# Optimization experiments

Measured on AMD Instinct MI355X. Metric: run time of the kernel, lower is better.

The kernel has to match this reference:

```python
import jax, jax.numpy as jnp
import numpy as np
from jax import lax

D_MODEL = 2048
D_STATE = 16
D_CONV = 4
B_SZ = 2
T_LEN = 2048


def setup_inputs() -> dict:
    key = jax.random.key(0)
    ks = jax.random.split(key, 8)
    x = jax.random.normal(ks[0], (B_SZ, T_LEN, D_MODEL), dtype=jnp.float32)
    h = jnp.zeros((B_SZ, D_MODEL, D_STATE), dtype=jnp.float32)
    norm_w = jnp.ones((D_MODEL,), dtype=jnp.float32)
    in_proj_w = jax.random.normal(ks[1], (2 * D_MODEL, D_MODEL), dtype=jnp.float32) * (D_MODEL ** -0.5)
    conv_w = jax.random.normal(ks[2], (D_MODEL, 1, D_CONV), dtype=jnp.float32) * 0.5
    conv_b = jnp.zeros((D_MODEL,), dtype=jnp.float32)
    x_proj_w = jax.random.normal(ks[3], (D_MODEL + 2 * D_STATE, D_MODEL), dtype=jnp.float32) * (D_MODEL ** -0.5)
    A_log = jnp.broadcast_to(jnp.log(jnp.arange(1, D_STATE + 1, dtype=jnp.float32))[None, :], (D_MODEL, D_STATE)).copy()
    D = jnp.ones((D_MODEL,), dtype=jnp.float32)
    out_proj_w = jax.random.normal(ks[4], (D_MODEL, D_MODEL), dtype=jnp.float32) * (D_MODEL ** -0.5)
    return {"x": x, "h": h, "norm_w": norm_w, "in_proj_w": in_proj_w,
            "conv_w": conv_w, "conv_b": conv_b, "x_proj_w": x_proj_w,
            "A_log": A_log, "D": D, "out_proj_w": out_proj_w}


def _rmsnorm(x, w, eps=1e-6):
    ms = jnp.mean(jnp.square(x.astype(jnp.float32)), axis=-1, keepdims=True)
    return (x * lax.rsqrt(ms + eps).astype(x.dtype)) * w.astype(x.dtype)


def reference(x, h, norm_w, in_proj_w, conv_w, conv_b, x_proj_w, A_log, D, out_proj_w):
    B, T, d_model = x.shape
    d_state = A_log.shape[1]
    residual = x
    x_normed = _rmsnorm(x, norm_w)
    xz = x_normed @ in_proj_w.T                      # (B, T, 2*d_model)
    x_branch, z = jnp.split(xz, 2, axis=-1)
    # depthwise causal conv1d: torch pads both sides by d_conv-1 then slices [:T],
    # equivalent to left-pad-only causal conv.
    xc = x_branch.transpose(0, 2, 1)                 # (B, d_model, T)
    xc = lax.conv_general_dilated(
        xc, conv_w, window_strides=(1,), padding=[(D_CONV - 1, 0)],
        dimension_numbers=("NCH", "OIH", "NCH"), feature_group_count=d_model)
    xc = xc + conv_b[None, :, None]
    x_ssm = jax.nn.silu(xc.transpose(0, 2, 1))       # (B, T, d_model)

    # SSM core
    proj = x_ssm @ x_proj_w.T                        # (B, T, d_model + 2*d_state)
    delta_raw = proj[..., :d_model]
    B_in = proj[..., d_model:d_model + d_state]
    C_in = proj[..., d_model + d_state:]
    delta = jax.nn.softplus(delta_raw)               # (B, T, d_model)
    A = -jnp.exp(A_log.astype(jnp.float32))          # (d_model, d_state)

    def step(h_c, inp):
        d_t, b_t, c_t, x_t = inp                     # (B,dm) (B,ds) (B,ds) (B,dm)
        A_bar = jnp.exp(d_t[:, :, None] * A[None])   # (B, dm, ds)
        h_c = A_bar * h_c + (d_t * x_t)[:, :, None] * b_t[:, None, :]
        y_t = jnp.einsum("bdn,bn->bd", h_c, c_t) + D * x_t
        return h_c, y_t

    xs = (delta.transpose(1, 0, 2), B_in.transpose(1, 0, 2),
          C_in.transpose(1, 0, 2), x_ssm.transpose(1, 0, 2))
    h_new, ys = lax.scan(step, h.astype(x.dtype), xs)
    y = ys.transpose(1, 0, 2)                        # (B, T, d_model)

    y = y * jax.nn.silu(z)
    out = residual + y @ out_proj_w.T
    return out, lax.stop_gradient(h_new)
```

## Files before the change

kernel.cpp:

```cpp
#include <hip/hip_runtime.h>
#include <cstdint>
#include <cstddef>


typedef __bf16 bf16_t;
typedef __attribute__((ext_vector_type(8))) __bf16 bf16x8;
typedef __attribute__((ext_vector_type(4))) __bf16 bf16x4;
typedef __attribute__((ext_vector_type(4))) float f32x4;

#define D_MODEL 2048
#define D_STATE 16
#define B_SZ 2
#define T_LEN 2048
#define N_ROWS (B_SZ * T_LEN)
#define N_PAD  2176
#define N_CHUNK 32
#define L_CHUNK (T_LEN / N_CHUNK)
#define LOG2E 1.4426950408889634f
#define KT 64
#define PANEL 32768

__device__ __forceinline__ size_t swz_idx(int row, int col) {
    return ((size_t)((row >> 4) * KT + (col >> 5)) << 9)
         + (size_t)(((row & 15) + (((col & 31) >> 3) << 4)) << 3) + (col & 7);
}

__global__ __launch_bounds__(256) void cast_weights(
    const float* __restrict__ w_in, const float* __restrict__ w_x,
    const float* __restrict__ w_out,
    bf16_t* __restrict__ W1s, bf16_t* __restrict__ W2s, bf16_t* __restrict__ W3s)
{
    int wv   = blockIdx.x * 4 + (threadIdx.x >> 6);
    int lane = threadIdx.x & 63;
    const float* src; bf16_t* dst; int nrows; int tile;
    if (wv < 16384)      { src = w_in;  dst = W1s; tile = wv;         nrows = 4096; }
    else if (wv < 25088) { src = w_x;   dst = W2s; tile = wv - 16384; nrows = 2080; }
    else                 { src = w_out; dst = W3s; tile = wv - 25088; nrows = 2048; }
    int r16 = tile >> 6, kt = tile & 63;
    int row = r16 * 16 + (lane & 15);
    int k0  = kt * 32 + (lane >> 4) * 8;
    f32x4 v0 = {0.f, 0.f, 0.f, 0.f}, v1 = v0;
    if (row < nrows) {
        v0 = *(const f32x4*)&src[(size_t)row * 2048 + k0];
        v1 = *(const f32x4*)&src[(size_t)row * 2048 + k0 + 4];
    }
    bf16x4 lo = __builtin_convertvector(v0, bf16x4);
    bf16x4 hi = __builtin_convertvector(v1, bf16x4);
    bf16x8 o;
    #pragma unroll
    for (int e = 0; e < 4; ++e) { o[e] = lo[e]; o[e + 4] = hi[e]; }
    *(bf16x8*)(dst + (size_t)tile * 512 + lane * 8) = o;
}

__global__ __launch_bounds__(256) void rmsnorm_swz(
    const float* __restrict__ x, const float* __restrict__ w,
    bf16_t* __restrict__ xn)
{
    int r16 = blockIdx.x;
    int tid = threadIdx.x;
    int wave = tid >> 6, lane = tid & 63;
    __shared__ float sc[16];
    #pragma unroll
    for (int rr = 0; rr < 4; ++rr) {
        int row = r16 * 16 + wave * 4 + rr;
        const float* xr = x + (size_t)row * 2048;
        float ss = 0.f;
        for (int i = lane * 4; i < 2048; i += 256) {
            f32x4 v = *(const f32x4*)&xr[i];
            ss += v[0]*v[0] + v[1]*v[1] + v[2]*v[2] + v[3]*v[3];
        }
        #pragma unroll
        for (int o = 32; o > 0; o >>= 1) ss += __shfl_down(ss, o, 64);
        if (lane == 0) sc[wave * 4 + rr] = rsqrtf(ss * (1.f / 2048.f) + 1e-6f);
    }
    __syncthreads();
    const size_t base = (size_t)r16 * PANEL;
    int m = lane & 15;
    int row = r16 * 16 + m;
    float s = sc[m];
    const float* xr = x + (size_t)row * 2048;
    for (int c = 0; c < 16; ++c) {
        int f  = (c * 256 + tid) * 8;
        int kt = f >> 9;
        int k  = kt * 32 + (lane >> 4) * 8;
        f32x4 v0 = *(const f32x4*)&xr[k];
        f32x4 v1 = *(const f32x4*)&xr[k + 4];
        f32x4 w0 = *(const f32x4*)&w[k];
        f32x4 w1 = *(const f32x4*)&w[k + 4];
        bf16x8 o;
        #pragma unroll
        for (int e = 0; e < 4; ++e) {
            o[e]     = (bf16_t)(v0[e] * s * w0[e]);
            o[e + 4] = (bf16_t)(v1[e] * s * w1[e]);
        }
        *(bf16x8*)(xn + base + f) = o;
    }
}

template<int MODE>
__global__ __launch_bounds__(256) void gemm_bt(
    const bf16_t* __restrict__ A, const bf16_t* __restrict__ B,
    float* __restrict__ out0, bf16_t* __restrict__ out1,
    const float* __restrict__ add)
{
    __shared__ __align__(16) float cs[32 * 132];
    const int tid = threadIdx.x;
    const int bm = blockIdx.x, bn = blockIdx.y;
    const int lane = tid & 63;
    const int wave = tid >> 6;
    const int wn = (wave >> 1) * 64;
    const int fr = lane & 15;
    const int quad = lane >> 4;

    const bf16_t* aB = A + (((size_t)(bm * 8 + (wave & 1) * 4) * KT) << 9) + lane * 8;
    const bf16_t* bB = B + (((size_t)(bn * 8 + (wave >> 1) * 4) * KT) << 9) + lane * 8;

    f32x4 acc[4][4];
    #pragma unroll
    for (int i = 0; i < 4; ++i)
        #pragma unroll
        for (int j = 0; j < 4; ++j) acc[i][j] = {0.f, 0.f, 0.f, 0.f};

    bf16x8 aC[4], bC[4];
    #pragma unroll
    for (int i = 0; i < 4; ++i) {
        aC[i] = *(const bf16x8*)(aB + (size_t)i * PANEL);
        bC[i] = *(const bf16x8*)(bB + (size_t)i * PANEL);
    }
    #pragma unroll 2
    for (int kt = 0; kt < KT; ++kt) {
        const int ktn = (kt < KT - 1) ? (kt + 1) : (KT - 1);
        bf16x8 aN[4], bN[4];
        #pragma unroll
        for (int i = 0; i < 4; ++i) {
            aN[i] = *(const bf16x8*)(aB + (size_t)i * PANEL + ((size_t)ktn << 9));
            bN[i] = *(const bf16x8*)(bB + (size_t)i * PANEL + ((size_t)ktn << 9));
        }
        #pragma unroll
        for (int i = 0; i < 4; ++i)
            #pragma unroll
            for (int j = 0; j < 4; ++j)
                acc[i][j] = __builtin_amdgcn_mfma_f32_16x16x32_bf16(
                    aC[i], bC[j], acc[i][j], 0, 0, 0);
        #pragma unroll
        for (int i = 0; i < 4; ++i) { aC[i] = aN[i]; bC[i] = bN[i]; }
    }

    const int lrow0 = (wave & 1) * 16 + quad * 4;
    const int lcol0 = wn + fr;
    for (int i = 0; i < 4; ++i) {
        __syncthreads();
        #pragma unroll
        for (int j = 0; j < 4; ++j)
            #pragma unroll
            for (int rr = 0; rr < 4; ++rr)
                cs[(lrow0 + rr) * 132 + lcol0 + j * 16] = acc[i][j][rr];
        __syncthreads();
        #pragma unroll
        for (int k = 0; k < 4; ++k) {
            int f4  = tid + k * 256;
            int row = f4 >> 5;
            int c4  = (f4 & 31) * 4;
            f32x4 v = *(const f32x4*)&cs[row * 132 + c4];
            int gr = bm * 128 + i * 16 + ((row < 16) ? row : (48 + row));
            int gc = bn * 128 + c4;
            if (MODE == 0) {
                if (bn < 16) {
                    *(f32x4*)&out0[(size_t)gr * 2048 + gc] = v;
                } else {
                    bf16x4 o;
                    #pragma unroll
                    for (int e = 0; e < 4; ++e) {
                        float s = v[e];
                        o[e] = (bf16_t)(s / (1.f + __expf(-s)));
                    }
                    *(bf16x4*)&out1[(size_t)gr * 2048 + (gc - 2048)] = o;
                }
            } else if (MODE == 1) {
                if (bn < 16) {
                    #pragma unroll
                    for (int e = 0; e < 4; ++e) {
                        float s = v[e];
                        v[e] = fmaxf(s, 0.f) + __logf(1.f + __expf(-fabsf(s)));
                    }
                }
                *(f32x4*)&out0[(size_t)gr * N_PAD + gc] = v;
            } else {
                f32x4 a4 = *(const f32x4*)&add[(size_t)gr * 2048 + gc];
                v = v + a4;
                *(f32x4*)&out0[(size_t)gr * 2048 + gc] = v;
            }
        }
    }
}

__global__ __launch_bounds__(256) void conv_silu_swz(
    const float* __restrict__ xb, const float* __restrict__ cw,
    const float* __restrict__ cb, bf16_t* __restrict__ xs_s)
{
    int id = blockIdx.x * 256 + threadIdx.x;
    int dq = id & 255;
    int t  = (id >> 8) & 2047;
    int b  = id >> 19;
    int d0 = dq * 8;
    f32x4 cwv[8];
    #pragma unroll
    for (int e = 0; e < 8; ++e) cwv[e] = *(const f32x4*)&cw[(d0 + e) * 4];
    float a[8];
    {
        f32x4 b0 = *(const f32x4*)&cb[d0], b1 = *(const f32x4*)&cb[d0 + 4];
        #pragma unroll
        for (int e = 0; e < 4; ++e) { a[e] = b0[e]; a[4 + e] = b1[e]; }
    }
    #pragma unroll
    for (int tap = 0; tap < 4; ++tap) {
        int tr = t - 3 + tap;
        if (tr >= 0) {
            const float* xr = xb + ((size_t)(b * 2048 + tr)) * 2048 + d0;
            f32x4 x0 = *(const f32x4*)xr, x1 = *(const f32x4*)(xr + 4);
            #pragma unroll
            for (int e = 0; e < 4; ++e) {
                a[e]     = fmaf(cwv[e][tap],     x0[e], a[e]);
                a[4 + e] = fmaf(cwv[4 + e][tap], x1[e], a[4 + e]);
            }
        }
    }
    bf16x8 o;
    #pragma unroll
    for (int e = 0; e < 8; ++e) {
        float s = a[e];
        o[e] = (bf16_t)(s / (1.f + __expf(-s)));
    }
    int row = b * 2048 + t;
    size_t off = ((size_t)((row >> 4) * KT + (dq >> 2)) << 9)
               + (size_t)(((row & 15) + ((dq & 3) << 4)) << 3);
    *(bf16x8*)(xs_s + off) = o;
}

#define PF 4

__device__ __forceinline__ size_t xs_off(int row, int ddo) {
    return ((size_t)(row >> 4) << 15) + (size_t)((row & 15) << 3) + ddo;
}

__global__ __launch_bounds__(256) void scan_phase1(
    const float* __restrict__ proj, const bf16_t* __restrict__ xs,
    const float* __restrict__ A_log,
    float* __restrict__ Aprod, float* __restrict__ hfin)
{
    int wi   = blockIdx.x * 4 + (threadIdx.x >> 6);
    int lane = threadIdx.x & 63;
    int nq   = lane & 3;
    int dsub = lane >> 2;
    int c  = wi & 31;
    int dg = (wi >> 5) & 127;
    int b  = wi >> 12;
    int dd = dg * 16 + dsub;
    const int ddo = ((dd >> 5) << 9) + (((dd & 31) >> 3) << 7) + (dd & 7);

    float A2[4], h[4], Ap[4];
    #pragma unroll
    for (int j = 0; j < 4; ++j) {
        A2[j] = -__expf(A_log[dd * D_STATE + nq * 4 + j]) * LOG2E;
        h[j] = 0.f; Ap[j] = 1.f;
    }
    const int t0 = c * L_CHUNK;
    const int tmax = t0 + L_CHUNK - 1;

    float p_da[PF], p_xv[PF];
    f32x4 p_B[PF];
    #pragma unroll
    for (int u = 0; u < PF; ++u) {
        int row = b * T_LEN + t0 + u;
        const float* pr = proj + (size_t)row * N_PAD;
        p_da[u] = pr[dd];
        p_xv[u] = (float)xs[xs_off(row, ddo)];
        p_B[u]  = *(const f32x4*)(pr + D_MODEL + nq * 4);
    }

    for (int it = 0; it < L_CHUNK; it += PF) {
        #pragma unroll
        for (int u = 0; u < PF; ++u) {
            int t = t0 + it + u;
            float da = p_da[u], xv = p_xv[u];
            f32x4 Bv = p_B[u];
            int tn = t + PF; tn = (tn > tmax) ? tmax : tn;
            {
                int row = b * T_LEN + tn;
                const float* pr = proj + (size_t)row * N_PAD;
                p_da[u] = pr[dd];
                p_xv[u] = (float)xs[xs_off(row, ddo)];
                p_B[u]  = *(const f32x4*)(pr + D_MODEL + nq * 4);
            }
            float dx = da * xv;
            #pragma unroll
            for (int j = 0; j < 4; ++j) {
                float a = exp2f(da * A2[j]);
                Ap[j] *= a;
                h[j] = fmaf(a, h[j], dx * Bv[j]);
            }
        }
    }
    size_t o = ((size_t)c * 4096 + b * 2048 + dd) * D_STATE + nq * 4;
    *(f32x4*)(Aprod + o) = f32x4{Ap[0], Ap[1], Ap[2], Ap[3]};
    *(f32x4*)(hfin  + o) = f32x4{h[0], h[1], h[2], h[3]};
}

__global__ __launch_bounds__(256) void scan_phase2(
    const float* __restrict__ h_in, const float* __restrict__ Aprod,
    float* __restrict__ hfin, float* __restrict__ h_out)
{
    int g = blockIdx.x * 256 + threadIdx.x;
    float h = h_in[g];
    for (int c = 0; c < N_CHUNK; ++c) {
        size_t o = (size_t)c * 65536 + g;
        float a   = Aprod[o];
        float loc = hfin[o];
        hfin[o] = h;
        h = fmaf(a, h, loc);
    }
    h_out[g] = h;
}

__global__ __launch_bounds__(256) void scan_phase3(
    const float* __restrict__ proj, const bf16_t* __restrict__ xs,
    const bf16_t* __restrict__ zg, const float* __restrict__ A_log,
    const float* __restrict__ Dv, const float* __restrict__ hinit,
    bf16_t* __restrict__ yg)
{
    int wi   = blockIdx.x * 4 + (threadIdx.x >> 6);
    int lane = threadIdx.x & 63;
    int nq   = lane & 3;
    int dsub = lane >> 2;
    int c  = wi & 31;
    int dg = (wi >> 5) & 127;
    int b  = wi >> 12;
    int dd = dg * 16 + dsub;
    const int ddo = ((dd >> 5) << 9) + (((dd & 31) >> 3) << 7) + (dd & 7);

    float A2[4], h[4];
    size_t o = ((size_t)c * 4096 + b * 2048 + dd) * D_STATE + nq * 4;
    #pragma unroll
    for (int j = 0; j < 4; ++j) {
        A2[j] = -__expf(A_log[dd * D_STATE + nq * 4 + j]) * LOG2E;
        h[j]  = hinit[o + j];
    }
    float Dd = Dv[dd];
    const int t0 = c * L_CHUNK;
    const int tmax = t0 + L_CHUNK - 1;

    float p_da[PF], p_xv[PF], p_sz[PF];
    f32x4 p_B[PF], p_C[PF];
    #pragma unroll
    for (int u = 0; u < PF; ++u) {
        int row = b * T_LEN + t0 + u;
        const float* pr = proj + (size_t)row * N_PAD;
        p_da[u] = pr[dd];
        p_xv[u] = (float)xs[xs_off(row, ddo)];
        p_sz[u] = (float)zg[(size_t)row * 2048 + dd];
        p_B[u]  = *(const f32x4*)(pr + D_MODEL + nq * 4);
        p_C[u]  = *(const f32x4*)(pr + D_MODEL + D_STATE + nq * 4);
    }

    for (int it = 0; it < L_CHUNK; it += PF) {
        #pragma unroll
        for (int u = 0; u < PF; ++u) {
            int t = t0 + it + u;
            float da = p_da[u], xv = p_xv[u], sz = p_sz[u];
            f32x4 Bv = p_B[u], Cv = p_C[u];
            int tn = t + PF; tn = (tn > tmax) ? tmax : tn;
            {
                int row = b * T_LEN + tn;
                const float* pr = proj + (size_t)row * N_PAD;
                p_da[u] = pr[dd];
                p_xv[u] = (float)xs[xs_off(row, ddo)];
                p_sz[u] = (float)zg[(size_t)row * 2048 + dd];
                p_B[u]  = *(const f32x4*)(pr + D_MODEL + nq * 4);
                p_C[u]  = *(const f32x4*)(pr + D_MODEL + D_STATE + nq * 4);
            }
            float dx = da * xv;
            float yp = 0.f;
            #pragma unroll
            for (int j = 0; j < 4; ++j) {
                float a = exp2f(da * A2[j]);
                h[j] = fmaf(a, h[j], dx * Bv[j]);
                yp = fmaf(h[j], Cv[j], yp);
            }
            yp += __shfl_xor(yp, 1, 64);
            yp += __shfl_xor(yp, 2, 64);
            if (nq == 0) {
                float y = fmaf(Dd, xv, yp);
                int row = b * T_LEN + t;
                yg[xs_off(row, ddo)] = (bf16_t)(y * sz);
            }
        }
    }
}

extern "C" void kernel_launch(void* const* d_in, const int* in_sizes, int n_in,
                              void* d_out, int out_size, void* d_ws, size_t ws_size,
                              hipStream_t stream)
{
    const float* x    = (const float*)d_in[0];
    const float* h0   = (const float*)d_in[1];
    const float* nw   = (const float*)d_in[2];
    const float* w_in = (const float*)d_in[3];
    const float* cw   = (const float*)d_in[4];
    const float* cb   = (const float*)d_in[5];
    const float* w_x  = (const float*)d_in[6];
    const float* alog = (const float*)d_in[7];
    const float* dv   = (const float*)d_in[8];
    const float* w_out= (const float*)d_in[9];
    float* out  = (float*)d_out;
    float* hout = out + (size_t)N_ROWS * D_MODEL;

    char* ws = (char*)d_ws;
    size_t off = 0;
    auto alloc = [&](size_t bytes) -> void* {
        void* p = ws + off;
        off += (bytes + 255) & ~(size_t)255;
        return p;
    };
    bf16_t* W1  = (bf16_t*)alloc((size_t)16384 * 512 * 2);
    bf16_t* W2  = (bf16_t*)alloc((size_t)8704 * 512 * 2);
    bf16_t* W3  = (bf16_t*)alloc((size_t)8192 * 512 * 2);
    bf16_t* XN  = (bf16_t*)alloc((size_t)N_ROWS * 2048 * 2);
    float*  XB  = (float*) alloc((size_t)N_ROWS * 2048 * 4);
    bf16_t* ZG  = (bf16_t*)alloc((size_t)N_ROWS * 2048 * 2);
    float*  PROJ= (float*) alloc((size_t)N_ROWS * N_PAD * 4);
    float* APROD= (float*) alloc((size_t)N_CHUNK * 4096 * D_STATE * 4);
    float* HFIN = (float*) alloc((size_t)N_CHUNK * 4096 * D_STATE * 4);
    bf16_t* XSb = W1;
    bf16_t* YG  = XN;

    cast_weights<<<8320, 256, 0, stream>>>(w_in, w_x, w_out, W1, W2, W3);

    rmsnorm_swz<<<256, 256, 0, stream>>>(x, nw, XN);
    gemm_bt<0><<<dim3(32, 32), 256, 0, stream>>>(XN, W1, XB, ZG, nullptr);
    conv_silu_swz<<<(B_SZ * T_LEN * 256) / 256, 256, 0, stream>>>(XB, cw, cb, XSb);
    gemm_bt<1><<<dim3(32, N_PAD / 128), 256, 0, stream>>>(XSb, W2, PROJ, nullptr, nullptr);
    scan_phase1<<<2048, 256, 0, stream>>>(PROJ, XSb, alog, APROD, HFIN);
    scan_phase2<<<256, 256, 0, stream>>>(h0, APROD, HFIN, hout);
    scan_phase3<<<2048, 256, 0, stream>>>(PROJ, XSb, ZG, alog, dv, HFIN, YG);
    gemm_bt<2><<<dim3(32, 16), 256, 0, stream>>>(YG, W3, out, nullptr, x);

    (void)in_sizes; (void)n_in; (void)out_size; (void)ws_size;
}
```

Baseline: 541.9 us.

## Rework GEMM to 2-wave 64x128 warp tiles, stage rmsnorm via LDS, retile conv

The GEMM now runs 128 threads per block, and each wave computes a 64x128 tile (4x8 MFMA fragments) instead of 32x64. This raises register-level reuse of the A and B fragments loaded from global memory, and the epilogue uses per-wave LDS staging with no block barriers. Rmsnorm reads x once into registers, writes normalized bf16 rows to LDS, then emits the swizzled layout from LDS instead of re-reading x from global. The conv kernel is remapped to the swizzled tile order so its writes are contiguous. The larger accumulator tile raises VGPR pressure and may lower occupancy, and fewer waves per block may hide memory latency less well.

```diff
diff --git a/kernel.cpp b/kernel.cpp
--- a/kernel.cpp
+++ b/kernel.cpp
@@ -19,11 +19,6 @@
 #define LOG2E 1.4426950408889634f
 #define KT 64
 #define PANEL 32768
-
-__device__ __forceinline__ size_t swz_idx(int row, int col) {
-    return ((size_t)((row >> 4) * KT + (col >> 5)) << 9)
-         + (size_t)(((row & 15) + (((col & 31) >> 3) << 4)) << 3) + (col & 7);
-}
 
 __global__ __launch_bounds__(256) void cast_weights(
     const float* __restrict__ w_in, const float* __restrict__ w_x,
@@ -56,113 +51,116 @@
     const float* __restrict__ x, const float* __restrict__ w,
     bf16_t* __restrict__ xn)
 {
+    __shared__ bf16_t st[16][2056];
     int r16 = blockIdx.x;
     int tid = threadIdx.x;
     int wave = tid >> 6, lane = tid & 63;
-    __shared__ float sc[16];
-    #pragma unroll
+
+    f32x4 wv[8];
+    #pragma unroll
+    for (int c = 0; c < 8; ++c) wv[c] = *(const f32x4*)&w[(c * 64 + lane) * 4];
+
     for (int rr = 0; rr < 4; ++rr) {
         int row = r16 * 16 + wave * 4 + rr;
         const float* xr = x + (size_t)row * 2048;
+        f32x4 vv[8];
         float ss = 0.f;
-        for (int i = lane * 4; i < 2048; i += 256) {
-            f32x4 v = *(const f32x4*)&xr[i];
-            ss += v[0]*v[0] + v[1]*v[1] + v[2]*v[2] + v[3]*v[3];
+        #pragma unroll
+        for (int c = 0; c < 8; ++c) {
+            vv[c] = *(const f32x4*)&xr[(c * 64 + lane) * 4];
+            ss += vv[c][0]*vv[c][0] + vv[c][1]*vv[c][1]
+                + vv[c][2]*vv[c][2] + vv[c][3]*vv[c][3];
         }
         #pragma unroll
         for (int o = 32; o > 0; o >>= 1) ss += __shfl_down(ss, o, 64);
-        if (lane == 0) sc[wave * 4 + rr] = rsqrtf(ss * (1.f / 2048.f) + 1e-6f);
+        float s = __shfl(ss, 0, 64);
+        s = rsqrtf(s * (1.f / 2048.f) + 1e-6f);
+        #pragma unroll
+        for (int c = 0; c < 8; ++c) {
+            bf16x4 o4;
+            #pragma unroll
+            for (int e = 0; e < 4; ++e) o4[e] = (bf16_t)(vv[c][e] * s * wv[c][e]);
+            *(bf16x4*)&st[wave * 4 + rr][(c * 64 + lane) * 4] = o4;
+        }
     }
     __syncthreads();
     const size_t base = (size_t)r16 * PANEL;
-    int m = lane & 15;
-    int row = r16 * 16 + m;
-    float s = sc[m];
-    const float* xr = x + (size_t)row * 2048;
+    #pragma unroll
     for (int c = 0; c < 16; ++c) {
         int f  = (c * 256 + tid) * 8;
         int kt = f >> 9;
-        int k  = kt * 32 + (lane >> 4) * 8;
-        f32x4 v0 = *(const f32x4*)&xr[k];
-        f32x4 v1 = *(const f32x4*)&xr[k + 4];
-        f32x4 w0 = *(const f32x4*)&w[k];
-        f32x4 w1 = *(const f32x4*)&w[k + 4];
-        bf16x8 o;
-        #pragma unroll
-        for (int e = 0; e < 4; ++e) {
-            o[e]     = (bf16_t)(v0[e] * s * w0[e]);
-            o[e + 4] = (bf16_t)(v1[e] * s * w1[e]);
-        }
-        *(bf16x8*)(xn + base + f) = o;
+        int off3 = (f & 511) >> 3;
+        int m = off3 & 15, q = off3 >> 4;
+        bf16x8 v = *(const bf16x8*)&st[m][kt * 32 + q * 8];
+        *(bf16x8*)(xn + base + f) = v;
     }
 }
 
 template<int MODE>
-__global__ __launch_bounds__(256) void gemm_bt(
+__global__ __launch_bounds__(128) void gemm_bt(
     const bf16_t* __restrict__ A, const bf16_t* __restrict__ B,
     float* __restrict__ out0, bf16_t* __restrict__ out1,
     const float* __restrict__ add)
 {
-    __shared__ __align__(16) float cs[32 * 132];
+    __shared__ __align__(16) float cs[2][16 * 132];
     const int tid = threadIdx.x;
     const int bm = blockIdx.x, bn = blockIdx.y;
     const int lane = tid & 63;
     const int wave = tid >> 6;
-    const int wn = (wave >> 1) * 64;
     const int fr = lane & 15;
     const int quad = lane >> 4;
 
-    const bf16_t* aB = A + (((size_t)(bm * 8 + (wave & 1) * 4) * KT) << 9) + lane * 8;
-    const bf16_t* bB = B + (((size_t)(bn * 8 + (wave >> 1) * 4) * KT) << 9) + lane * 8;
-
-    f32x4 acc[4][4];
+    const bf16_t* aB = A + (((size_t)(bm * 8 + wave * 4) * KT) << 9) + lane * 8;
+    const bf16_t* bB = B + (((size_t)(bn * 8) * KT) << 9) + lane * 8;
+
+    f32x4 acc[4][8];
     #pragma unroll
     for (int i = 0; i < 4; ++i)
         #pragma unroll
-        for (int j = 0; j < 4; ++j) acc[i][j] = {0.f, 0.f, 0.f, 0.f};
-
-    bf16x8 aC[4], bC[4];
-    #pragma unroll
-    for (int i = 0; i < 4; ++i) {
-        aC[i] = *(const bf16x8*)(aB + (size_t)i * PANEL);
-        bC[i] = *(const bf16x8*)(bB + (size_t)i * PANEL);
-    }
+        for (int j = 0; j < 8; ++j) acc[i][j] = {0.f, 0.f, 0.f, 0.f};
+
+    bf16x8 aC[4], bC[8];
+    #pragma unroll
+    for (int i = 0; i < 4; ++i) aC[i] = *(const bf16x8*)(aB + (size_t)i * PANEL);
+    #pragma unroll
+    for (int j = 0; j < 8; ++j) bC[j] = *(const bf16x8*)(bB + (size_t)j * PANEL);
+
     #pragma unroll 2
     for (int kt = 0; kt < KT; ++kt) {
         const int ktn = (kt < KT - 1) ? (kt + 1) : (KT - 1);
-        bf16x8 aN[4], bN[4];
-        #pragma unroll
-        for (int i = 0; i < 4; ++i) {
+        bf16x8 aN[4], bN[8];
+        #pragma unroll
+        for (int i = 0; i < 4; ++i)
             aN[i] = *(const bf16x8*)(aB + (size_t)i * PANEL + ((size_t)ktn << 9));
-            bN[i] = *(const bf16x8*)(bB + (size_t)i * PANEL + ((size_t)ktn << 9));
-        }
+        #pragma unroll
+        for (int j = 0; j < 8; ++j)
+            bN[j] = *(const bf16x8*)(bB + (size_t)j * PANEL + ((size_t)ktn << 9));
         #pragma unroll
         for (int i = 0; i < 4; ++i)
             #pragma unroll
-            for (int j = 0; j < 4; ++j)
+            for (int j = 0; j < 8; ++j)
                 acc[i][j] = __builtin_amdgcn_mfma_f32_16x16x32_bf16(
                     aC[i], bC[j], acc[i][j], 0, 0, 0);
         #pragma unroll
-        for (int i = 0; i < 4; ++i) { aC[i] = aN[i]; bC[i] = bN[i]; }
-    }
-
-    const int lrow0 = (wave & 1) * 16 + quad * 4;
-    const int lcol0 = wn + fr;
+        for (int i = 0; i < 4; ++i) aC[i] = aN[i];
+        #pragma unroll
+        for (int j = 0; j < 8; ++j) bC[j] = bN[j];
+    }
+
+    float* csw = cs[wave];
     for (int i = 0; i < 4; ++i) {
-        __syncthreads();
-        #pragma unroll
-        for (int j = 0; j < 4; ++j)
+        #pragma unroll
+        for (int j = 0; j < 8; ++j)
             #pragma unroll
             for (int rr = 0; rr < 4; ++rr)
-                cs[(lrow0 + rr) * 132 + lcol0 + j * 16] = acc[i][j][rr];
-        __syncthreads();
-        #pragma unroll
-        for (int k = 0; k < 4; ++k) {
-            int f4  = tid + k * 256;
-            int row = f4 >> 5;
-            int c4  = (f4 & 31) * 4;
-            f32x4 v = *(const f32x4*)&cs[row * 132 + c4];
-            int gr = bm * 128 + i * 16 + ((row < 16) ? row : (48 + row));
+                csw[(quad * 4 + rr) * 132 + j * 16 + fr] = acc[i][j][rr];
+        #pragma unroll
+        for (int s = 0; s < 8; ++s) {
+            int t   = lane + s * 64;
+            int row = t >> 5;
+            int c4  = (t & 31) * 4;
+            f32x4 v = *(const f32x4*)&csw[row * 132 + c4];
+            int gr = bm * 128 + wave * 64 + i * 16 + row;
             int gc = bn * 128 + c4;
             if (MODE == 0) {
                 if (bn < 16) {
@@ -171,8 +169,8 @@
                     bf16x4 o;
                     #pragma unroll
                     for (int e = 0; e < 4; ++e) {
-                        float s = v[e];
-                        o[e] = (bf16_t)(s / (1.f + __expf(-s)));
+                        float sv = v[e];
+                        o[e] = (bf16_t)(sv / (1.f + __expf(-sv)));
                     }
                     *(bf16x4*)&out1[(size_t)gr * 2048 + (gc - 2048)] = o;
                 }
@@ -180,8 +178,8 @@
                 if (bn < 16) {
                     #pragma unroll
                     for (int e = 0; e < 4; ++e) {
-                        float s = v[e];
-                        v[e] = fmaxf(s, 0.f) + __logf(1.f + __expf(-fabsf(s)));
+                        float sv = v[e];
+                        v[e] = fmaxf(sv, 0.f) + __logf(1.f + __expf(-fabsf(sv)));
                     }
                 }
                 *(f32x4*)&out0[(size_t)gr * N_PAD + gc] = v;
@@ -198,25 +196,30 @@
     const float* __restrict__ xb, const float* __restrict__ cw,
     const float* __restrict__ cb, bf16_t* __restrict__ xs_s)
 {
-    int id = blockIdx.x * 256 + threadIdx.x;
-    int dq = id & 255;
-    int t  = (id >> 8) & 2047;
-    int b  = id >> 19;
-    int d0 = dq * 8;
-    f32x4 cwv[8];
-    #pragma unroll
-    for (int e = 0; e < 8; ++e) cwv[e] = *(const f32x4*)&cw[(d0 + e) * 4];
+    int tile = blockIdx.x * 4 + (threadIdx.x >> 6);
+    int lane = threadIdx.x & 63;
+    int r16  = tile >> 6;
+    int dt   = tile & 63;
+    int m    = lane & 15;
+    int d0   = dt * 32 + (lane >> 4) * 8;
+    int row  = r16 * 16 + m;
+    int t    = row & 2047;
+
     float a[8];
     {
         f32x4 b0 = *(const f32x4*)&cb[d0], b1 = *(const f32x4*)&cb[d0 + 4];
         #pragma unroll
         for (int e = 0; e < 4; ++e) { a[e] = b0[e]; a[4 + e] = b1[e]; }
     }
+    f32x4 cwv[8];
+    #pragma unroll
+    for (int e = 0; e < 8; ++e) cwv[e] = *(const f32x4*)&cw[(d0 + e) * 4];
+
     #pragma unroll
     for (int tap = 0; tap < 4; ++tap) {
         int tr = t - 3 + tap;
         if (tr >= 0) {
-            const float* xr = xb + ((size_t)(b * 2048 + tr)) * 2048 + d0;
+            const float* xr = xb + ((size_t)(row - 3 + tap)) * 2048 + d0;
             f32x4 x0 = *(const f32x4*)xr, x1 = *(const f32x4*)(xr + 4);
             #pragma unroll
             for (int e = 0; e < 4; ++e) {
@@ -231,10 +234,7 @@
         float s = a[e];
         o[e] = (bf16_t)(s / (1.f + __expf(-s)));
     }
-    int row = b * 2048 + t;
-    size_t off = ((size_t)((row >> 4) * KT + (dq >> 2)) << 9)
-               + (size_t)(((row & 15) + ((dq & 3) << 4)) << 3);
-    *(bf16x8*)(xs_s + off) = o;
+    *(bf16x8*)(xs_s + (size_t)tile * 512 + lane * 8) = o;
 }
 
 #define PF 4
@@ -436,13 +436,13 @@
     cast_weights<<<8320, 256, 0, stream>>>(w_in, w_x, w_out, W1, W2, W3);
 
     rmsnorm_swz<<<256, 256, 0, stream>>>(x, nw, XN);
-    gemm_bt<0><<<dim3(32, 32), 256, 0, stream>>>(XN, W1, XB, ZG, nullptr);
-    conv_silu_swz<<<(B_SZ * T_LEN * 256) / 256, 256, 0, stream>>>(XB, cw, cb, XSb);
-    gemm_bt<1><<<dim3(32, N_PAD / 128), 256, 0, stream>>>(XSb, W2, PROJ, nullptr, nullptr);
+    gemm_bt<0><<<dim3(32, 32), 128, 0, stream>>>(XN, W1, XB, ZG, nullptr);
+    conv_silu_swz<<<4096, 256, 0, stream>>>(XB, cw, cb, XSb);
+    gemm_bt<1><<<dim3(32, 17), 128, 0, stream>>>(XSb, W2, PROJ, nullptr, nullptr);
     scan_phase1<<<2048, 256, 0, stream>>>(PROJ, XSb, alog, APROD, HFIN);
     scan_phase2<<<256, 256, 0, stream>>>(h0, APROD, HFIN, hout);
     scan_phase3<<<2048, 256, 0, stream>>>(PROJ, XSb, ZG, alog, dv, HFIN, YG);
-    gemm_bt<2><<<dim3(32, 16), 256, 0, stream>>>(YG, W3, out, nullptr, x);
+    gemm_bt<2><<<dim3(32, 16), 128, 0, stream>>>(YG, W3, out, nullptr, x);
 
     (void)in_sizes; (void)n_in; (void)out_size; (void)ws_size;
 }
```

After: 594.5 us. 1.1x slower.
